# Kernel tuning notes

Measured on AMD Instinct MI355X. Metric: run time of the kernel, lower is better.

Reference implementation:

```python
import jax, jax.numpy as jnp
import numpy as np

D_EMB = 256


def setup_inputs() -> dict:
    key = jax.random.key(0)
    ks = jax.random.split(key, 7)
    B, S, d = 4, 4096, D_EMB
    scale = 1.0 / np.sqrt(d)
    return {
        "x": jax.random.normal(ks[0], (B, S, d), jnp.float32),
        "Wqkv": jax.random.normal(ks[1], (d, 3 * d), jnp.float32) * scale,
        "bqkv": jax.random.normal(ks[2], (3 * d,), jnp.float32) * 0.02,
        "Wproj": jax.random.normal(ks[3], (d, d), jnp.float32) * scale,
        "bproj": jax.random.normal(ks[4], (d,), jnp.float32) * 0.02,
        "Wfc": jax.random.normal(ks[5], (d, 1), jnp.float32) * scale,
        "bfc": jax.random.normal(ks[6], (1,), jnp.float32) * 0.02,
    }


def reference(x, Wqkv, bqkv, Wproj, bproj, Wfc, bfc):
    # qkv projection: [B,S,3d] -> split into q,k,v [B,S,d]
    qkv = x @ Wqkv + bqkv
    q, k, v = jnp.split(qkv, 3, axis=2)
    # full attention scores [B,S,S]; note: original applies NO 1/sqrt(d)
    # scaling (dead branch in source), 'traditional' softmax over last dim
    attn_scores = jnp.einsum("bqd,bkd->bqk", q, k)
    attn_weights = jax.nn.softmax(attn_scores, axis=-1)
    y = jnp.einsum("bqk,bkd->bqd", attn_weights, v)
    y = y @ Wproj + bproj
    out = y @ Wfc + bfc  # [B,S,1]
    return out
```

## Files before the change

kernel.cpp:

```cpp
#include <hip/hip_runtime.h>
#include <hip/hip_bf16.h>

#define BQ 4
#define SQ 4096
#define DQ 256
#define N3 768
#define KBLK 64
#define NITER (SQ / KBLK)
#define KHALF (NITER / 2)

typedef __attribute__((ext_vector_type(8))) _Float16 f16x8;
typedef __attribute__((ext_vector_type(4))) float f32x4;
typedef __attribute__((ext_vector_type(4))) unsigned int u32x4;

__device__ __forceinline__ short f2h(float f) {
  _Float16 h = (_Float16)f;
  union { _Float16 h; short s; } v; v.h = h;
  return v.s;
}

__device__ __forceinline__ void gload16(const void* g, void* lds) {
  __builtin_amdgcn_global_load_lds(
      (const __attribute__((address_space(1))) unsigned int*)g,
      (__attribute__((address_space(3))) unsigned int*)lds, 16, 0, 0);
}

__global__ void wcomb_kernel(const float* __restrict__ Wproj,
                             const float* __restrict__ bproj,
                             const float* __restrict__ Wfc,
                             const float* __restrict__ bfc,
                             float* __restrict__ Wc) {
  __shared__ float wf[256];
  const int t = threadIdx.x;
  wf[t] = Wfc[t];
  __syncthreads();
  float acc = 0.f;
  for (int j = 0; j < 256; ++j) acc += Wproj[(size_t)t * 256 + j] * wf[j];
  Wc[t] = acc;
  if (t == 0) {
    float c = bfc[0];
    for (int j = 0; j < 256; ++j) c += bproj[j] * wf[j];
    Wc[256] = c;
  }
}

__global__ void wconv_kernel(const float* __restrict__ Wqkv,
                             short* __restrict__ W16T) {
  const int n = blockIdx.x, k = threadIdx.x;
  W16T[(size_t)n * 256 + k] = f2h(Wqkv[(size_t)k * N3 + n]);
}

__global__ __launch_bounds__(1024, 4) void qkv_kernel(
    const float* __restrict__ x, const short* __restrict__ W16T,
    const float* __restrict__ bqkv, const float* __restrict__ Wc,
    short* __restrict__ Qb, short* __restrict__ Kb, float* __restrict__ u) {
  __shared__ short xs[64][264];
  __shared__ short ws[2][64][256];
  __shared__ float u_red[4][4][16];
  const int t = threadIdx.x;
  const int l = t & 63, w = t >> 6;
  const int lr = l & 15, lg = l >> 4;
  const int mq = w >> 2, nq = w & 3;
  const int Mbase = blockIdx.x * 64;

#define STAGE_W(BUF, NT)                                                      \
  {                                                                           \
    _Pragma("unroll") for (int i = 0; i < 2; ++i) {                           \
      const int n = w * 4 + i * 2 + (l >> 5);                                 \
      const int gc = (l & 31) ^ (n & 7);                                      \
      gload16(W16T + (size_t)((NT)*64 + n) * 256 + gc * 8,                    \
              &ws[BUF][w * 4 + i * 2][0]);                                    \
    }                                                                         \
  }

  STAGE_W(0, 0);

  {
    const int m = t >> 4, kc = (t & 15) * 16;
    const float* src = x + (size_t)(Mbase + m) * DQ + kc;
    short tmp[16];
#pragma unroll
    for (int i = 0; i < 16; ++i) tmp[i] = f2h(src[i]);
    *(u32x4*)&xs[m][kc] = *(u32x4*)&tmp[0];
    *(u32x4*)&xs[m][kc + 8] = *(u32x4*)&tmp[8];
  }

  float bias_qk[8], bias_u[4], wc_u[4];
#pragma unroll
  for (int i = 0; i < 8; ++i) bias_qk[i] = bqkv[i * 64 + nq * 16 + lr];
#pragma unroll
  for (int i = 0; i < 4; ++i) {
    bias_u[i] = bqkv[512 + i * 64 + nq * 16 + lr];
    wc_u[i] = Wc[i * 64 + nq * 16 + lr];
  }

  __syncthreads();

  unsigned qksto[8][2];
  float upart[4] = {0.f, 0.f, 0.f, 0.f};

#pragma unroll
  for (int nt = 0; nt < 12; ++nt) {
    const int cur = nt & 1;
    if (nt + 1 < 12) {
      STAGE_W(cur ^ 1, nt + 1);
      asm volatile("s_waitcnt vmcnt(2)" ::: "memory");
    } else {
      asm volatile("s_waitcnt vmcnt(0)" ::: "memory");
    }
    __builtin_amdgcn_s_barrier();
    __builtin_amdgcn_sched_barrier(0);

    f32x4 acc = {};
    const char* wR = (const char*)&ws[cur][nq * 16 + lr][0];
#pragma unroll
    for (int kk = 0; kk < 8; ++kk) {
      f16x8 af = *(f16x8*)&xs[mq * 16 + lr][kk * 32 + lg * 8];
      f16x8 bfr = *(const f16x8*)(wR + (((4 * kk + lg) ^ (lr & 7)) << 4));
      acc = __builtin_amdgcn_mfma_f32_16x16x32_f16(af, bfr, acc, 0, 0, 0);
    }
    if (nt < 8) {
      unsigned s0 = (unsigned short)f2h(acc[0] + bias_qk[nt]);
      unsigned s1 = (unsigned short)f2h(acc[1] + bias_qk[nt]);
      unsigned s2 = (unsigned short)f2h(acc[2] + bias_qk[nt]);
      unsigned s3 = (unsigned short)f2h(acc[3] + bias_qk[nt]);
      qksto[nt][0] = s0 | (s1 << 16);
      qksto[nt][1] = s2 | (s3 << 16);
    } else {
#pragma unroll
      for (int r = 0; r < 4; ++r) upart[r] += (acc[r] + bias_u[nt - 8]) * wc_u[nt - 8];
    }
    __builtin_amdgcn_s_barrier();
  }

#pragma unroll
  for (int nt = 0; nt < 8; ++nt) {
    const int col = nt * 64 + nq * 16 + lr;
#pragma unroll
    for (int r = 0; r < 4; ++r) {
      const int row = Mbase + mq * 16 + lg * 4 + r;
      const short sv = (short)((qksto[nt][r >> 1] >> ((r & 1) * 16)) & 0xFFFF);
      if (col < 256) Qb[(size_t)row * DQ + col] = sv;
      else           Kb[(size_t)row * DQ + (col - 256)] = sv;
    }
  }

#pragma unroll
  for (int mask = 1; mask <= 8; mask <<= 1)
#pragma unroll
    for (int r = 0; r < 4; ++r) upart[r] += __shfl_xor(upart[r], mask, 64);
  if (lr == 0) {
#pragma unroll
    for (int r = 0; r < 4; ++r) u_red[mq][nq][lg * 4 + r] = upart[r];
  }
  __syncthreads();
  if (t < 64)
    u[Mbase + t] = u_red[t >> 4][0][t & 15] + u_red[t >> 4][1][t & 15] +
                   u_red[t >> 4][2][t & 15] + u_red[t >> 4][3][t & 15];
#undef STAGE_W
}

__global__ __launch_bounds__(256, 2) void attn_kernel(
    const short* __restrict__ Qb, const short* __restrict__ Kb,
    const float* __restrict__ u, float* __restrict__ Pm,
    float* __restrict__ Pd, float* __restrict__ Pn) {
  __shared__ short Ks[2][64][256];
  __shared__ __align__(16) float u_lds[2048];
  __shared__ float Mrg[2][2][32][3];

  const int t = threadIdx.x;
  const int l = t & 63, w = t >> 6;
  const int lr = l & 15, lg = l >> 4;
  const int qg = w >> 1, h = w & 1;
  const int bid = blockIdx.x;
  const int b = bid & 3;
  const int half = (bid >> 2) & 1;
  const int qbase = (bid >> 3) * 64;

  const short* kbase = Kb + ((size_t)b * SQ + (size_t)half * (SQ / 2)) * DQ;
  const float* ubase = u + (size_t)b * SQ + half * (SQ / 2);

#define STAGE(BUF, KB)                                                      \
  {                                                                         \
    _Pragma("unroll") for (int i = 0; i < 8; ++i) {                         \
      const int kr = w * 16 + i * 2 + (l >> 5);                             \
      const int gc = (l & 31) ^ (kr & 7);                                   \
      gload16(kbase + (size_t)((KB)*64 + kr) * DQ + gc * 8,                 \
              &Ks[BUF][w * 16 + i * 2][0]);                                 \
    }                                                                       \
  }

  STAGE(0, 0);
  gload16(ubase + w * 256 + (l << 2), &u_lds[w * 256]);
  gload16(ubase + (4 + w) * 256 + (l << 2), &u_lds[(4 + w) * 256]);

  f16x8 qf[2][8];
#pragma unroll
  for (int mm = 0; mm < 2; ++mm) {
    const short* qptr = Qb + (size_t)(b * SQ + qbase + qg * 32 + mm * 16 + lr) * DQ;
#pragma unroll
    for (int kk = 0; kk < 8; ++kk)
      qf[mm][kk] = *(const f16x8*)(qptr + kk * 32 + lg * 8);
  }

  float m_run[2] = {-1e30f, -1e30f};
  float num[2] = {0.f, 0.f}, den[2] = {0.f, 0.f};

  __syncthreads();

  for (int kb = 0; kb < KHALF; ++kb) {
    const int cur = kb & 1;
    if (kb + 1 < KHALF) {
      STAGE(cur ^ 1, kb + 1);
      asm volatile("s_waitcnt vmcnt(8)" ::: "memory");
    } else {
      asm volatile("s_waitcnt vmcnt(0)" ::: "memory");
    }
    __builtin_amdgcn_s_barrier();
    __builtin_amdgcn_sched_barrier(0);

    f32x4 sA[2][2] = {}, sB[2][2] = {};
    __builtin_amdgcn_s_setprio(1);
#pragma unroll
    for (int kc = 0; kc < 2; ++kc) {
      const char* kR = (const char*)&Ks[cur][h * 32 + kc * 16 + lr][0];
#pragma unroll
      for (int kk = 0; kk < 4; ++kk) {
        f16x8 kf = *(const f16x8*)(kR + (((4 * kk + lg) ^ (lr & 7)) << 4));
        sA[kc][0] = __builtin_amdgcn_mfma_f32_16x16x32_f16(kf, qf[0][kk], sA[kc][0], 0, 0, 0);
        sA[kc][1] = __builtin_amdgcn_mfma_f32_16x16x32_f16(kf, qf[1][kk], sA[kc][1], 0, 0, 0);
      }
#pragma unroll
      for (int kk = 4; kk < 8; ++kk) {
        f16x8 kf = *(const f16x8*)(kR + (((4 * kk + lg) ^ (lr & 7)) << 4));
        sB[kc][0] = __builtin_amdgcn_mfma_f32_16x16x32_f16(kf, qf[0][kk], sB[kc][0], 0, 0, 0);
        sB[kc][1] = __builtin_amdgcn_mfma_f32_16x16x32_f16(kf, qf[1][kk], sB[kc][1], 0, 0, 0);
      }
    }
    __builtin_amdgcn_s_setprio(0);
    f32x4 s[2][2];
#pragma unroll
    for (int kc = 0; kc < 2; ++kc)
#pragma unroll
      for (int mm = 0; mm < 2; ++mm)
#pragma unroll
        for (int r = 0; r < 4; ++r) s[kc][mm][r] = sA[kc][mm][r] + sB[kc][mm][r];

    bool over = false;
#pragma unroll
    for (int kc = 0; kc < 2; ++kc)
#pragma unroll
      for (int mm = 0; mm < 2; ++mm)
#pragma unroll
        for (int r = 0; r < 4; ++r) over = over || (s[kc][mm][r] > m_run[mm] + 8.f);
    if (__any(over)) {
#pragma unroll
      for (int mm = 0; mm < 2; ++mm) {
        float mt = s[0][mm][0];
#pragma unroll
        for (int r = 1; r < 4; ++r) mt = fmaxf(mt, s[0][mm][r]);
#pragma unroll
        for (int r = 0; r < 4; ++r) mt = fmaxf(mt, s[1][mm][r]);
        mt = fmaxf(mt, __shfl_xor(mt, 16, 64));
        mt = fmaxf(mt, __shfl_xor(mt, 32, 64));
        const float mn = fmaxf(m_run[mm], mt);
        const float sc = __expf(m_run[mm] - mn);
        m_run[mm] = mn;
        num[mm] *= sc;
        den[mm] *= sc;
      }
    }
#pragma unroll
    for (int kc = 0; kc < 2; ++kc) {
      const f32x4 uv = *(const f32x4*)&u_lds[kb * 64 + h * 32 + kc * 16 + lg * 4];
#pragma unroll
      for (int mm = 0; mm < 2; ++mm)
#pragma unroll
        for (int r = 0; r < 4; ++r) {
          const float p = __expf(s[kc][mm][r] - m_run[mm]);
          den[mm] += p;
          num[mm] += p * uv[r];
        }
    }
    __builtin_amdgcn_s_barrier();
  }

#pragma unroll
  for (int mm = 0; mm < 2; ++mm) {
    num[mm] += __shfl_xor(num[mm], 16, 64);
    num[mm] += __shfl_xor(num[mm], 32, 64);
    den[mm] += __shfl_xor(den[mm], 16, 64);
    den[mm] += __shfl_xor(den[mm], 32, 64);
  }
  if (lg == 0) {
#pragma unroll
    for (int mm = 0; mm < 2; ++mm) {
      Mrg[qg][h][mm * 16 + lr][0] = m_run[mm];
      Mrg[qg][h][mm * 16 + lr][1] = den[mm];
      Mrg[qg][h][mm * 16 + lr][2] = num[mm];
    }
  }
  __syncthreads();

  if (t < 64) {
    const int row = t & 31, qg2 = t >> 5;
    const float m0 = Mrg[qg2][0][row][0], m1 = Mrg[qg2][1][row][0];
    const float M = fmaxf(m0, m1);
    const float e0 = __expf(m0 - M), e1 = __expf(m1 - M);
    const float dt = e0 * Mrg[qg2][0][row][1] + e1 * Mrg[qg2][1][row][1];
    const float nt = e0 * Mrg[qg2][0][row][2] + e1 * Mrg[qg2][1][row][2];
    const size_t idx = (size_t)half * (BQ * SQ) + (size_t)b * SQ + qbase + qg2 * 32 + row;
    Pm[idx] = M; Pd[idx] = dt; Pn[idx] = nt;
  }
#undef STAGE
}

__global__ void merge_kernel(const float* __restrict__ Pm,
                             const float* __restrict__ Pd,
                             const float* __restrict__ Pn,
                             const float* __restrict__ Wc,
                             float* __restrict__ out) {
  const int gid = blockIdx.x * 256 + threadIdx.x;
  const float m0 = Pm[gid], m1 = Pm[BQ * SQ + gid];
  const float M = fmaxf(m0, m1);
  const float e0 = __expf(m0 - M), e1 = __expf(m1 - M);
  const float den = e0 * Pd[gid] + e1 * Pd[BQ * SQ + gid];
  const float num = e0 * Pn[gid] + e1 * Pn[BQ * SQ + gid];
  out[gid] = num / den + Wc[256];
}

extern "C" void kernel_launch(void* const* d_in, const int* in_sizes, int n_in,
                              void* d_out, int out_size, void* d_ws, size_t ws_size,
                              hipStream_t stream) {
  const float* x     = (const float*)d_in[0];
  const float* Wqkv  = (const float*)d_in[1];
  const float* bqkv  = (const float*)d_in[2];
  const float* Wproj = (const float*)d_in[3];
  const float* bproj = (const float*)d_in[4];
  const float* Wfc   = (const float*)d_in[5];
  const float* bfc   = (const float*)d_in[6];
  float* out = (float*)d_out;

  const size_t SEG = (size_t)BQ * SQ * DQ * 2;
  char* wsb = (char*)d_ws;
  short* Qb   = (short*)(wsb);
  short* Kb   = (short*)(wsb + SEG);
  char* base  = wsb + 2 * SEG;
  float* Wc   = (float*)(base);
  float* u    = (float*)(base + 4096);
  short* W16T = (short*)(base + 4096 + 65536);
  float* Pm   = (float*)(base + 4096 + 65536 + 393216);
  float* Pd   = Pm + 2 * BQ * SQ;
  float* Pn   = Pd + 2 * BQ * SQ;

  wcomb_kernel<<<1, 256, 0, stream>>>(Wproj, bproj, Wfc, bfc, Wc);
  wconv_kernel<<<N3, 256, 0, stream>>>(Wqkv, W16T);
  qkv_kernel<<<256, 1024, 0, stream>>>(x, W16T, bqkv, Wc, Qb, Kb, u);
  attn_kernel<<<512, 256, 0, stream>>>(Qb, Kb, u, Pm, Pd, Pn);
  merge_kernel<<<BQ * SQ / 256, 256, 0, stream>>>(Pm, Pd, Pn, Wc, out);
}
```

Before: 104.4 us.

## Split attention key tiles across more waves, fold log2e into K, tile weight transpose

The attention kernel doubles its block to 8 waves, so each wave handles 16 key rows per tile instead of 32. The per-block softmax merge now combines four partial states. The log2(e) factor is folded into the fp16 K projection so the softmax can use exp2 instead of exp, and the lazy-rescale threshold is adjusted to match. The Wqkv transpose-convert kernel now uses an LDS-tiled transpose for coalesced reads. Together these are meant to raise occupancy and latency hiding, trimming exponential cost and uncoalesced weight loads, at the price of more cross-wave merging and a change in fp16 rounding of K.

Measured after the change: 105.8 us. About the same (+1.3%).

```diff
diff --git a/kernel.cpp b/kernel.cpp
--- a/kernel.cpp
+++ b/kernel.cpp
@@ -8,6 +8,8 @@
 #define KBLK 64
 #define NITER (SQ / KBLK)
 #define KHALF (NITER / 2)
+#define LOG2E 1.44269504f
+#define THR2 11.5415603f
 
 typedef __attribute__((ext_vector_type(8))) _Float16 f16x8;
 typedef __attribute__((ext_vector_type(4))) float f32x4;
@@ -46,8 +48,18 @@
 
 __global__ void wconv_kernel(const float* __restrict__ Wqkv,
                              short* __restrict__ W16T) {
-  const int n = blockIdx.x, k = threadIdx.x;
-  W16T[(size_t)n * 256 + k] = f2h(Wqkv[(size_t)k * N3 + n]);
+  __shared__ float tile[64][65];
+  const int nb = blockIdx.x * 64;
+  const int kb = blockIdx.y * 64;
+  const int t = threadIdx.x;
+  const int tr = t >> 6, tc = t & 63;
+#pragma unroll
+  for (int i = 0; i < 16; ++i)
+    tile[tr + i * 4][tc] = Wqkv[(size_t)(kb + tr + i * 4) * N3 + nb + tc];
+  __syncthreads();
+#pragma unroll
+  for (int i = 0; i < 16; ++i)
+    W16T[(size_t)(nb + tr + i * 4) * 256 + kb + tc] = f2h(tile[tc][tr + i * 4]);
 }
 
 __global__ __launch_bounds__(1024, 4) void qkv_kernel(
@@ -120,10 +132,11 @@
       acc = __builtin_amdgcn_mfma_f32_16x16x32_f16(af, bfr, acc, 0, 0, 0);
     }
     if (nt < 8) {
-      unsigned s0 = (unsigned short)f2h(acc[0] + bias_qk[nt]);
-      unsigned s1 = (unsigned short)f2h(acc[1] + bias_qk[nt]);
-      unsigned s2 = (unsigned short)f2h(acc[2] + bias_qk[nt]);
-      unsigned s3 = (unsigned short)f2h(acc[3] + bias_qk[nt]);
+      const float sc = (nt < 4) ? 1.f : LOG2E;
+      unsigned s0 = (unsigned short)f2h((acc[0] + bias_qk[nt]) * sc);
+      unsigned s1 = (unsigned short)f2h((acc[1] + bias_qk[nt]) * sc);
+      unsigned s2 = (unsigned short)f2h((acc[2] + bias_qk[nt]) * sc);
+      unsigned s3 = (unsigned short)f2h((acc[3] + bias_qk[nt]) * sc);
       qksto[nt][0] = s0 | (s1 << 16);
       qksto[nt][1] = s2 | (s3 << 16);
     } else {
@@ -160,18 +173,18 @@
 #undef STAGE_W
 }
 
-__global__ __launch_bounds__(256, 2) void attn_kernel(
+__global__ __launch_bounds__(512, 4) void attn_kernel(
     const short* __restrict__ Qb, const short* __restrict__ Kb,
     const float* __restrict__ u, float* __restrict__ Pm,
     float* __restrict__ Pd, float* __restrict__ Pn) {
   __shared__ short Ks[2][64][256];
   __shared__ __align__(16) float u_lds[2048];
-  __shared__ float Mrg[2][2][32][3];
+  __shared__ float Mrg[2][4][32][3];
 
   const int t = threadIdx.x;
   const int l = t & 63, w = t >> 6;
   const int lr = l & 15, lg = l >> 4;
-  const int qg = w >> 1, h = w & 1;
+  const int qg = w >> 2, h = w & 3;
   const int bid = blockIdx.x;
   const int b = bid & 3;
   const int half = (bid >> 2) & 1;
@@ -182,17 +195,16 @@
 
 #define STAGE(BUF, KB)                                                      \
   {                                                                         \
-    _Pragma("unroll") for (int i = 0; i < 8; ++i) {                         \
-      const int kr = w * 16 + i * 2 + (l >> 5);                             \
+    _Pragma("unroll") for (int i = 0; i < 4; ++i) {                         \
+      const int kr = w * 8 + i * 2 + (l >> 5);                              \
       const int gc = (l & 31) ^ (kr & 7);                                   \
       gload16(kbase + (size_t)((KB)*64 + kr) * DQ + gc * 8,                 \
-              &Ks[BUF][w * 16 + i * 2][0]);                                 \
+              &Ks[BUF][w * 8 + i * 2][0]);                                  \
     }                                                                       \
   }
 
   STAGE(0, 0);
   gload16(ubase + w * 256 + (l << 2), &u_lds[w * 256]);
-  gload16(ubase + (4 + w) * 256 + (l << 2), &u_lds[(4 + w) * 256]);
 
   f16x8 qf[2][8];
 #pragma unroll
@@ -212,72 +224,49 @@
     const int cur = kb & 1;
     if (kb + 1 < KHALF) {
       STAGE(cur ^ 1, kb + 1);
-      asm volatile("s_waitcnt vmcnt(8)" ::: "memory");
+      asm volatile("s_waitcnt vmcnt(4)" ::: "memory");
     } else {
       asm volatile("s_waitcnt vmcnt(0)" ::: "memory");
     }
     __builtin_amdgcn_s_barrier();
     __builtin_amdgcn_sched_barrier(0);
 
-    f32x4 sA[2][2] = {}, sB[2][2] = {};
+    const char* kR = (const char*)&Ks[cur][h * 16 + lr][0];
+    f32x4 s[2] = {};
     __builtin_amdgcn_s_setprio(1);
 #pragma unroll
-    for (int kc = 0; kc < 2; ++kc) {
-      const char* kR = (const char*)&Ks[cur][h * 32 + kc * 16 + lr][0];
-#pragma unroll
-      for (int kk = 0; kk < 4; ++kk) {
-        f16x8 kf = *(const f16x8*)(kR + (((4 * kk + lg) ^ (lr & 7)) << 4));
-        sA[kc][0] = __builtin_amdgcn_mfma_f32_16x16x32_f16(kf, qf[0][kk], sA[kc][0], 0, 0, 0);
-        sA[kc][1] = __builtin_amdgcn_mfma_f32_16x16x32_f16(kf, qf[1][kk], sA[kc][1], 0, 0, 0);
-      }
-#pragma unroll
-      for (int kk = 4; kk < 8; ++kk) {
-        f16x8 kf = *(const f16x8*)(kR + (((4 * kk + lg) ^ (lr & 7)) << 4));
-        sB[kc][0] = __builtin_amdgcn_mfma_f32_16x16x32_f16(kf, qf[0][kk], sB[kc][0], 0, 0, 0);
-        sB[kc][1] = __builtin_amdgcn_mfma_f32_16x16x32_f16(kf, qf[1][kk], sB[kc][1], 0, 0, 0);
-      }
+    for (int kk = 0; kk < 8; ++kk) {
+      f16x8 kf = *(const f16x8*)(kR + (((4 * kk + lg) ^ (lr & 7)) << 4));
+      s[0] = __builtin_amdgcn_mfma_f32_16x16x32_f16(kf, qf[0][kk], s[0], 0, 0, 0);
+      s[1] = __builtin_amdgcn_mfma_f32_16x16x32_f16(kf, qf[1][kk], s[1], 0, 0, 0);
     }
     __builtin_amdgcn_s_setprio(0);
-    f32x4 s[2][2];
-#pragma unroll
-    for (int kc = 0; kc < 2; ++kc)
-#pragma unroll
-      for (int mm = 0; mm < 2; ++mm)
-#pragma unroll
-        for (int r = 0; r < 4; ++r) s[kc][mm][r] = sA[kc][mm][r] + sB[kc][mm][r];
 
     bool over = false;
 #pragma unroll
-    for (int kc = 0; kc < 2; ++kc)
-#pragma unroll
-      for (int mm = 0; mm < 2; ++mm)
-#pragma unroll
-        for (int r = 0; r < 4; ++r) over = over || (s[kc][mm][r] > m_run[mm] + 8.f);
+    for (int mm = 0; mm < 2; ++mm)
+#pragma unroll
+      for (int r = 0; r < 4; ++r) over = over || (s[mm][r] > m_run[mm] + THR2);
     if (__any(over)) {
 #pragma unroll
       for (int mm = 0; mm < 2; ++mm) {
-        float mt = s[0][mm][0];
-#pragma unroll
-        for (int r = 1; r < 4; ++r) mt = fmaxf(mt, s[0][mm][r]);
-#pragma unroll
-        for (int r = 0; r < 4; ++r) mt = fmaxf(mt, s[1][mm][r]);
+        float mt = fmaxf(fmaxf(s[mm][0], s[mm][1]), fmaxf(s[mm][2], s[mm][3]));
         mt = fmaxf(mt, __shfl_xor(mt, 16, 64));
         mt = fmaxf(mt, __shfl_xor(mt, 32, 64));
         const float mn = fmaxf(m_run[mm], mt);
-        const float sc = __expf(m_run[mm] - mn);
+        const float sc = exp2f(m_run[mm] - mn);
         m_run[mm] = mn;
         num[mm] *= sc;
         den[mm] *= sc;
       }
     }
-#pragma unroll
-    for (int kc = 0; kc < 2; ++kc) {
-      const f32x4 uv = *(const f32x4*)&u_lds[kb * 64 + h * 32 + kc * 16 + lg * 4];
+    {
+      const f32x4 uv = *(const f32x4*)&u_lds[kb * 64 + h * 16 + lg * 4];
 #pragma unroll
       for (int mm = 0; mm < 2; ++mm)
 #pragma unroll
         for (int r = 0; r < 4; ++r) {
-          const float p = __expf(s[kc][mm][r] - m_run[mm]);
+          const float p = exp2f(s[mm][r] - m_run[mm]);
           den[mm] += p;
           num[mm] += p * uv[r];
         }
@@ -304,12 +293,18 @@
 
   if (t < 64) {
     const int row = t & 31, qg2 = t >> 5;
-    const float m0 = Mrg[qg2][0][row][0], m1 = Mrg[qg2][1][row][0];
-    const float M = fmaxf(m0, m1);
-    const float e0 = __expf(m0 - M), e1 = __expf(m1 - M);
-    const float dt = e0 * Mrg[qg2][0][row][1] + e1 * Mrg[qg2][1][row][1];
-    const float nt = e0 * Mrg[qg2][0][row][2] + e1 * Mrg[qg2][1][row][2];
-    const size_t idx = (size_t)half * (BQ * SQ) + (size_t)b * SQ + qbase + qg2 * 32 + row;
+    float M = Mrg[qg2][0][row][0];
+#pragma unroll
+    for (int hh = 1; hh < 4; ++hh) M = fmaxf(M, Mrg[qg2][hh][row][0]);
+    float dt = 0.f, nt = 0.f;
+#pragma unroll
+    for (int hh = 0; hh < 4; ++hh) {
+      const float e = exp2f(Mrg[qg2][hh][row][0] - M);
+      dt += e * Mrg[qg2][hh][row][1];
+      nt += e * Mrg[qg2][hh][row][2];
+    }
+    const size_t idx = (size_t)half * (BQ * SQ) + (size_t)b * SQ + qbase + row +
+                       qg2 * 32;
     Pm[idx] = M; Pd[idx] = dt; Pn[idx] = nt;
   }
 #undef STAGE
@@ -323,7 +318,7 @@
   const int gid = blockIdx.x * 256 + threadIdx.x;
   const float m0 = Pm[gid], m1 = Pm[BQ * SQ + gid];
   const float M = fmaxf(m0, m1);
-  const float e0 = __expf(m0 - M), e1 = __expf(m1 - M);
+  const float e0 = exp2f(m0 - M), e1 = exp2f(m1 - M);
   const float den = e0 * Pd[gid] + e1 * Pd[BQ * SQ + gid];
   const float num = e0 * Pn[gid] + e1 * Pn[BQ * SQ + gid];
   out[gid] = num / den + Wc[256];
@@ -354,8 +349,8 @@
   float* Pn   = Pd + 2 * BQ * SQ;
 
   wcomb_kernel<<<1, 256, 0, stream>>>(Wproj, bproj, Wfc, bfc, Wc);
-  wconv_kernel<<<N3, 256, 0, stream>>>(Wqkv, W16T);
+  wconv_kernel<<<dim3(12, 4), 256, 0, stream>>>(Wqkv, W16T);
   qkv_kernel<<<256, 1024, 0, stream>>>(x, W16T, bqkv, Wc, Qb, Kb, u);
-  attn_kernel<<<512, 256, 0, stream>>>(Qb, Kb, u, Pm, Pd, Pn);
+  attn_kernel<<<512, 512, 0, stream>>>(Qb, Kb, u, Pm, Pd, Pn);
   merge_kernel<<<BQ * SQ / 256, 256, 0, stream>>>(Pm, Pd, Pn, Wc, out);
 }
```

## Fold log2e into K, use exp2 in softmax, merge prep kernels, simplify score accumulation

Applied to the files above, without the earlier changes.

K is pre-scaled by log2(e) when stored in the QKV kernel, so every softmax exponent becomes a native exp2 and the rescale threshold is raised to match. The two weight-prep kernels are merged into one launch with a tiled LDS transpose for the fp16 weight conversion. The score accumulation now uses a single accumulator chain per tile instead of two split halves, and the row max is computed once and reused. Swizzle offsets are hoisted out of the loop. Risks: longer MFMA dependency chains and a small fp16 rounding change from scaling K before conversion.

After: 93.78 us. 10.2% less time.

```diff
diff --git a/kernel.cpp b/kernel.cpp
--- a/kernel.cpp
+++ b/kernel.cpp
@@ -8,6 +8,8 @@
 #define KBLK 64
 #define NITER (SQ / KBLK)
 #define KHALF (NITER / 2)
+#define LOG2E 1.44269504f
+#define THR2 11.5415603f
 
 typedef __attribute__((ext_vector_type(8))) _Float16 f16x8;
 typedef __attribute__((ext_vector_type(4))) float f32x4;
@@ -25,29 +27,37 @@
       (__attribute__((address_space(3))) unsigned int*)lds, 16, 0, 0);
 }
 
-__global__ void wcomb_kernel(const float* __restrict__ Wproj,
-                             const float* __restrict__ bproj,
-                             const float* __restrict__ Wfc,
-                             const float* __restrict__ bfc,
-                             float* __restrict__ Wc) {
-  __shared__ float wf[256];
+__global__ __launch_bounds__(256) void prep_kernel(
+    const float* __restrict__ Wqkv, const float* __restrict__ Wproj,
+    const float* __restrict__ bproj, const float* __restrict__ Wfc,
+    const float* __restrict__ bfc, short* __restrict__ W16T,
+    float* __restrict__ Wc) {
   const int t = threadIdx.x;
-  wf[t] = Wfc[t];
-  __syncthreads();
-  float acc = 0.f;
-  for (int j = 0; j < 256; ++j) acc += Wproj[(size_t)t * 256 + j] * wf[j];
-  Wc[t] = acc;
-  if (t == 0) {
-    float c = bfc[0];
-    for (int j = 0; j < 256; ++j) c += bproj[j] * wf[j];
-    Wc[256] = c;
-  }
-}
-
-__global__ void wconv_kernel(const float* __restrict__ Wqkv,
-                             short* __restrict__ W16T) {
-  const int n = blockIdx.x, k = threadIdx.x;
-  W16T[(size_t)n * 256 + k] = f2h(Wqkv[(size_t)k * N3 + n]);
+  if (blockIdx.x == 48) {
+    __shared__ float wf[256];
+    wf[t] = Wfc[t];
+    __syncthreads();
+    float acc = 0.f;
+    for (int j = 0; j < 256; ++j) acc += Wproj[(size_t)t * 256 + j] * wf[j];
+    Wc[t] = acc;
+    if (t == 0) {
+      float c = bfc[0];
+      for (int j = 0; j < 256; ++j) c += bproj[j] * wf[j];
+      Wc[256] = c;
+    }
+    return;
+  }
+  __shared__ float tile[64][65];
+  const int nb = (blockIdx.x % 12) * 64;
+  const int kb = (blockIdx.x / 12) * 64;
+  const int tr = t >> 6, tc = t & 63;
+#pragma unroll
+  for (int i = 0; i < 16; ++i)
+    tile[tr + i * 4][tc] = Wqkv[(size_t)(kb + tr + i * 4) * N3 + nb + tc];
+  __syncthreads();
+#pragma unroll
+  for (int i = 0; i < 16; ++i)
+    W16T[(size_t)(nb + tr + i * 4) * 256 + kb + tc] = f2h(tile[tc][tr + i * 4]);
 }
 
 __global__ __launch_bounds__(1024, 4) void qkv_kernel(
@@ -120,10 +130,11 @@
       acc = __builtin_amdgcn_mfma_f32_16x16x32_f16(af, bfr, acc, 0, 0, 0);
     }
     if (nt < 8) {
-      unsigned s0 = (unsigned short)f2h(acc[0] + bias_qk[nt]);
-      unsigned s1 = (unsigned short)f2h(acc[1] + bias_qk[nt]);
-      unsigned s2 = (unsigned short)f2h(acc[2] + bias_qk[nt]);
-      unsigned s3 = (unsigned short)f2h(acc[3] + bias_qk[nt]);
+      const float sc = (nt < 4) ? 1.f : LOG2E;
+      unsigned s0 = (unsigned short)f2h((acc[0] + bias_qk[nt]) * sc);
+      unsigned s1 = (unsigned short)f2h((acc[1] + bias_qk[nt]) * sc);
+      unsigned s2 = (unsigned short)f2h((acc[2] + bias_qk[nt]) * sc);
+      unsigned s3 = (unsigned short)f2h((acc[3] + bias_qk[nt]) * sc);
       qksto[nt][0] = s0 | (s1 << 16);
       qksto[nt][1] = s2 | (s3 << 16);
     } else {
@@ -203,6 +214,10 @@
       qf[mm][kk] = *(const f16x8*)(qptr + kk * 32 + lg * 8);
   }
 
+  int koff[8];
+#pragma unroll
+  for (int kk = 0; kk < 8; ++kk) koff[kk] = ((4 * kk + lg) ^ (lr & 7)) << 4;
+
   float m_run[2] = {-1e30f, -1e30f};
   float num[2] = {0.f, 0.f}, den[2] = {0.f, 0.f};
 
@@ -219,52 +234,36 @@
     __builtin_amdgcn_s_barrier();
     __builtin_amdgcn_sched_barrier(0);
 
-    f32x4 sA[2][2] = {}, sB[2][2] = {};
+    f32x4 s[2][2] = {};
     __builtin_amdgcn_s_setprio(1);
 #pragma unroll
     for (int kc = 0; kc < 2; ++kc) {
       const char* kR = (const char*)&Ks[cur][h * 32 + kc * 16 + lr][0];
 #pragma unroll
-      for (int kk = 0; kk < 4; ++kk) {
-        f16x8 kf = *(const f16x8*)(kR + (((4 * kk + lg) ^ (lr & 7)) << 4));
-        sA[kc][0] = __builtin_amdgcn_mfma_f32_16x16x32_f16(kf, qf[0][kk], sA[kc][0], 0, 0, 0);
-        sA[kc][1] = __builtin_amdgcn_mfma_f32_16x16x32_f16(kf, qf[1][kk], sA[kc][1], 0, 0, 0);
+      for (int kk = 0; kk < 8; ++kk) {
+        f16x8 kf = *(const f16x8*)(kR + koff[kk]);
+        s[kc][0] = __builtin_amdgcn_mfma_f32_16x16x32_f16(kf, qf[0][kk], s[kc][0], 0, 0, 0);
+        s[kc][1] = __builtin_amdgcn_mfma_f32_16x16x32_f16(kf, qf[1][kk], s[kc][1], 0, 0, 0);
       }
-#pragma unroll
-      for (int kk = 4; kk < 8; ++kk) {
-        f16x8 kf = *(const f16x8*)(kR + (((4 * kk + lg) ^ (lr & 7)) << 4));
-        sB[kc][0] = __builtin_amdgcn_mfma_f32_16x16x32_f16(kf, qf[0][kk], sB[kc][0], 0, 0, 0);
-        sB[kc][1] = __builtin_amdgcn_mfma_f32_16x16x32_f16(kf, qf[1][kk], sB[kc][1], 0, 0, 0);
-      }
     }
     __builtin_amdgcn_s_setprio(0);
-    f32x4 s[2][2];
-#pragma unroll
-    for (int kc = 0; kc < 2; ++kc)
-#pragma unroll
-      for (int mm = 0; mm < 2; ++mm)
-#pragma unroll
-        for (int r = 0; r < 4; ++r) s[kc][mm][r] = sA[kc][mm][r] + sB[kc][mm][r];
-
-    bool over = false;
-#pragma unroll
-    for (int kc = 0; kc < 2; ++kc)
-#pragma unroll
-      for (int mm = 0; mm < 2; ++mm)
-#pragma unroll
-        for (int r = 0; r < 4; ++r) over = over || (s[kc][mm][r] > m_run[mm] + 8.f);
+
+    float mx[2];
+#pragma unroll
+    for (int mm = 0; mm < 2; ++mm)
+      mx[mm] = fmaxf(fmaxf(fmaxf(s[0][mm][0], s[0][mm][1]),
+                           fmaxf(s[0][mm][2], s[0][mm][3])),
+                     fmaxf(fmaxf(s[1][mm][0], s[1][mm][1]),
+                           fmaxf(s[1][mm][2], s[1][mm][3])));
+    const bool over = (mx[0] > m_run[0] + THR2) || (mx[1] > m_run[1] + THR2);
     if (__any(over)) {
 #pragma unroll
       for (int mm = 0; mm < 2; ++mm) {
-        float mt = s[0][mm][0];
-#pragma unroll
-        for (int r = 1; r < 4; ++r) mt = fmaxf(mt, s[0][mm][r]);
-#pragma unroll
-        for (int r = 0; r < 4; ++r) mt = fmaxf(mt, s[1][mm][r]);
+        float mt = mx[mm];
         mt = fmaxf(mt, __shfl_xor(mt, 16, 64));
         mt = fmaxf(mt, __shfl_xor(mt, 32, 64));
         const float mn = fmaxf(m_run[mm], mt);
-        const float sc = __expf(m_run[mm] - mn);
+        const float sc = __builtin_amdgcn_exp2f(m_run[mm] - mn);
         m_run[mm] = mn;
         num[mm] *= sc;
         den[mm] *= sc;
@@ -277,7 +276,7 @@
       for (int mm = 0; mm < 2; ++mm)
 #pragma unroll
         for (int r = 0; r < 4; ++r) {
-          const float p = __expf(s[kc][mm][r] - m_run[mm]);
+          const float p = __builtin_amdgcn_exp2f(s[kc][mm][r] - m_run[mm]);
           den[mm] += p;
           num[mm] += p * uv[r];
         }
@@ -306,7 +305,8 @@
     const int row = t & 31, qg2 = t >> 5;
     const float m0 = Mrg[qg2][0][row][0], m1 = Mrg[qg2][1][row][0];
     const float M = fmaxf(m0, m1);
-    const float e0 = __expf(m0 - M), e1 = __expf(m1 - M);
+    const float e0 = __builtin_amdgcn_exp2f(m0 - M);
+    const float e1 = __builtin_amdgcn_exp2f(m1 - M);
     const float dt = e0 * Mrg[qg2][0][row][1] + e1 * Mrg[qg2][1][row][1];
     const float nt = e0 * Mrg[qg2][0][row][2] + e1 * Mrg[qg2][1][row][2];
     const size_t idx = (size_t)half * (BQ * SQ) + (size_t)b * SQ + qbase + qg2 * 32 + row;
@@ -323,7 +323,8 @@
   const int gid = blockIdx.x * 256 + threadIdx.x;
   const float m0 = Pm[gid], m1 = Pm[BQ * SQ + gid];
   const float M = fmaxf(m0, m1);
-  const float e0 = __expf(m0 - M), e1 = __expf(m1 - M);
+  const float e0 = __builtin_amdgcn_exp2f(m0 - M);
+  const float e1 = __builtin_amdgcn_exp2f(m1 - M);
   const float den = e0 * Pd[gid] + e1 * Pd[BQ * SQ + gid];
   const float num = e0 * Pn[gid] + e1 * Pn[BQ * SQ + gid];
   out[gid] = num / den + Wc[256];
@@ -353,8 +354,7 @@
   float* Pd   = Pm + 2 * BQ * SQ;
   float* Pn   = Pd + 2 * BQ * SQ;
 
-  wcomb_kernel<<<1, 256, 0, stream>>>(Wproj, bproj, Wfc, bfc, Wc);
-  wconv_kernel<<<N3, 256, 0, stream>>>(Wqkv, W16T);
+  prep_kernel<<<49, 256, 0, stream>>>(Wqkv, Wproj, bproj, Wfc, bfc, W16T, Wc);
   qkv_kernel<<<256, 1024, 0, stream>>>(x, W16T, bqkv, Wc, Qb, Kb, u);
   attn_kernel<<<512, 256, 0, stream>>>(Qb, Kb, u, Pm, Pd, Pn);
   merge_kernel<<<BQ * SQ / 256, 256, 0, stream>>>(Pm, Pd, Pn, Wc, out);
```
